# Kernel optimization log

Hardware: AMD Instinct MI355X
Metric: run time of the kernel (lower is better)

Reference implementation:

```python
import jax, jax.numpy as jnp
import numpy as np
import math
jax.config.update('jax_enable_x64', True)

# ---- camera constants (match init_kwargs) ----
WAVELENGTHS = np.array([632e-9, 550e-9, 450e-9])
FOCAL_LENGTH = 50e-3
FOCAL_DEPTH = 1.7
MIN_DEPTH, MAX_DEPTH = 1.0, 5.0
N_DEPTHS = 16
IMAGE_SIZE = 384
MASK_SIZE = 2048
MASK_DIAMETER = 2.5e-3
PIXEL_PITCH = 6.45e-6
BATCH = 2
SENSOR_DIST = 1.0 / (1.0 / FOCAL_LENGTH - 1.0 / FOCAL_DEPTH)
MASK_PITCH = MASK_DIAMETER / MASK_SIZE
EPS = 1e-3


def _j1(x):
    # Bessel J1, Numerical Recipes rational approximation (double precision, ~1e-8 rel err)
    x = np.asarray(x, dtype=np.float64)
    ax = np.abs(x)
    y = x * x
    p1 = x * (72362614232.0 + y * (-7895059235.0 + y * (242396853.1 + y * (-2972611.439 + y * (15704.48260 + y * (-30.16036606))))))
    q1 = 144725228442.0 + y * (2300535178.0 + y * (18583304.74 + y * (99447.43394 + y * (376.9991397 + y))))
    small = p1 / q1
    axs = np.maximum(ax, 1e-300)
    z = 8.0 / axs
    y2 = z * z
    xx = ax - 2.356194491
    p2 = 1.0 + y2 * (0.183105e-2 + y2 * (-0.3516396496e-4 + y2 * (0.2457520174e-5 + y2 * (-0.240337019e-6))))
    q2 = 0.04687499995 + y2 * (-0.2002690873e-3 + y2 * (0.8449199096e-5 + y2 * (-0.88228987e-6 + y2 * 0.105787412e-6)))
    big = np.sqrt(0.636619772 / axs) * (np.cos(xx) * p2 - z * np.sin(xx) * q2) * np.sign(x)
    return np.where(ax < 8.0, small, big)


def _precompute():
    # scene distances: inverse-perspective sampling (ips_to_metric)
    d = np.linspace(0.0, 1.0, N_DEPTHS)
    scene_z = 1.0 / (d * (1.0 / MAX_DEPTH - 1.0 / MIN_DEPTH) + 1.0 / MIN_DEPTH)
    wl = WAVELENGTHS.reshape(-1, 1, 1)
    # --- precompute_H ---
    cy = PIXEL_PITCH * np.arange(1, IMAGE_SIZE // 2 + 1, dtype=np.float64).reshape(-1, 1)
    cx = PIXEL_PITCH * np.arange(1, IMAGE_SIZE // 2 + 1, dtype=np.float64).reshape(1, -1)
    rho_sampling = np.sqrt(cy ** 2 + cx ** 2)[None] / (wl * SENSOR_DIST)  # [3, H/2, W/2]
    rho_grid = math.sqrt(2) * PIXEL_PITCH * (np.arange(-1, IMAGE_SIZE // 2 + 1, dtype=np.float64) + 0.5)
    rho_grid = rho_grid.reshape(1, -1) / (WAVELENGTHS.reshape(-1, 1) * SENSOR_DIST)  # [3, R]
    r = MASK_PITCH * np.linspace(1, MASK_SIZE / 2, MASK_SIZE // 2).reshape(1, -1, 1)  # [1, M, 1]
    rg = rho_grid[:, None, :]  # [3, 1, R]
    denom = 2.0 * np.pi * rg
    safe = np.where(denom == 0.0, 1.0, denom)
    J = np.where(rg == 0.0, 0.5 * r ** 2, r * _j1(denom * r) / safe)  # [3, M, R]
    H = np.concatenate([J[:, 0:1, :], J[:, 1:, :] - J[:, :-1, :]], axis=1)  # [3, M, R]
    # --- pointsource_inputfield1d ---
    z = scene_z.reshape(1, -1, 1)
    rr = MASK_PITCH * np.linspace(1, MASK_SIZE / 2, MASK_SIZE // 2).reshape(1, 1, -1)
    k = 2.0 * np.pi / wl
    sqrt_z_r = np.sqrt(z ** 2 + rr ** 2)
    amp = z / wl / sqrt_z_r ** 2
    amp = amp / amp.max()
    phase = k * (sqrt_z_r - z)
    sqrt_r_d = np.sqrt(FOCAL_DEPTH ** 2 + rr ** 2)
    phase = phase - k * (sqrt_r_d - FOCAL_DEPTH)
    return (jnp.asarray(H), jnp.asarray(rho_grid), jnp.asarray(rho_sampling),
            jnp.asarray(amp), jnp.asarray(phase))


def setup_inputs() -> dict:
    key = jax.random.key(0)
    k1, k2, k3 = jax.random.split(key, 3)
    H, rho_grid, rho_sampling, prop_amplitude, prop_phase = _precompute()
    img = jax.random.uniform(k1, (BATCH, 3, IMAGE_SIZE, IMAGE_SIZE), dtype=jnp.float32)
    depthmap = jax.random.uniform(k2, (BATCH, 1, IMAGE_SIZE, IMAGE_SIZE), dtype=jnp.float32)
    # micron-scale DOE heightmap (learned parameter in the original)
    heightmap1d = jax.random.uniform(k3, (MASK_SIZE // 2,), dtype=jnp.float64) * 1e-6
    return {"img": img, "depthmap": depthmap, "heightmap1d": heightmap1d,
            "prop_amplitude": prop_amplitude, "prop_phase": prop_phase,
            "H": H, "rho_grid": rho_grid, "rho_sampling": rho_sampling,
            "occlusion": 1}


def reference(img, depthmap, heightmap1d, prop_amplitude, prop_phase, H, rho_grid, rho_sampling, occlusion):
    wl = jnp.asarray(WAVELENGTHS).reshape(-1, 1, 1)  # [3,1,1] float64
    # refractive index (Cauchy fit) and heightmap -> phase delay
    n_idx = 1.5375 + 0.00829045 / (wl * 1e6) ** 2 - 0.000211046 / (wl * 1e6) ** 4
    phase = 2.0 * jnp.pi / wl * (n_idx - 1.0) * heightmap1d.reshape(1, 1, -1) + prop_phase  # [3,D,M]
    # 1D PSF via Hankel transform (double precision)
    real = jnp.einsum('wdm,wmr->wdr', prop_amplitude * jnp.cos(phase), H)
    imag = jnp.einsum('wdm,wmr->wdr', prop_amplitude * jnp.sin(phase), H)
    psf1d = (2.0 * jnp.pi / (wl * SENSOR_DIST)) ** 2 * (real ** 2 + imag ** 2)  # [3,D,R]
    # interpolate radial PSF onto the 2D pixel rho grid (per wavelength)
    hh = IMAGE_SIZE // 2
    def interp_wl(grid, vals, samp):  # grid [R], vals [D,R], samp [hh,hh]
        return jax.vmap(lambda v: jnp.interp(samp.reshape(-1), grid, v))(vals)
    psf_rd = jax.vmap(interp_wl)(rho_grid, psf1d, rho_sampling)  # [3,D,hh*hh]
    psf_rd = jnp.maximum(psf_rd, 0.0).astype(jnp.float32).reshape(3, N_DEPTHS, hh, hh)
    # copy_quadruple: mirror quadrant to full image
    q = jnp.concatenate([jnp.flip(psf_rd, axis=-2), psf_rd], axis=-2)
    psf = jnp.concatenate([jnp.flip(q, axis=-1), q], axis=-1)  # [3,D,H,W]
    psf = jnp.fft.fftshift(psf, axes=(-2, -1))[None]  # [1,3,D,H,W]
    psf = psf / jnp.sum(psf, axis=(-2, -1), keepdims=True)  # normalize_psf
    # depthmap -> binary layered depth, volume
    idx = jnp.clip(jnp.floor(depthmap * N_DEPTHS).astype(jnp.int32), 0, N_DEPTHS - 1)  # [B,1,H,W]
    layered = (idx[:, :, None, :, :] == jnp.arange(N_DEPTHS).reshape(1, 1, -1, 1, 1)).astype(jnp.float32)
    volume = layered * img[:, :, None]  # [B,3,D,H,W]
    scale = volume.max()
    volume = volume / scale
    S = volume.shape[-2:]
    Fpsf = jnp.fft.rfft2(psf)
    blur = lambda a: jnp.fft.irfft2(jnp.fft.rfft2(a) * Fpsf, s=S)
    if occlusion:
        blurred_alpha = blur(layered)          # [B,3,D,H,W]
        blurred_volume = blur(volume)
        cumsum_alpha = jnp.flip(jnp.cumsum(jnp.flip(layered, axis=-3), axis=-3), axis=-3)
        blurred_cumsum = blur(cumsum_alpha)
        blurred_volume = blurred_volume / (blurred_cumsum + EPS)
        blurred_alpha = blurred_alpha / (blurred_cumsum + EPS)
        # over_op: front-to-back transmittance
        t = jnp.cumprod(1.0 - blurred_alpha, axis=-3)
        over = jnp.concatenate([jnp.ones_like(t[..., :1, :, :]), t[..., :-1, :, :]], axis=-3)
        captimg = jnp.sum(over * blurred_volume, axis=-3)
    else:
        captimg = jnp.sum(blur(volume), axis=-3)
    return scale * captimg  # [B,3,H,W]
```

## Files before the change

kernel.cpp:

```cpp
#include <hip/hip_runtime.h>
#include <math.h>

#define ND 16
#define NSZ 384
#define NHALF 192
#define NPIX 147456
#define QPIX 36864
#define MS2 1024
#define NG 194
#define EPSV 0.001f

__device__ __forceinline__ double ld64(const void* p, long i, int f){
  return f ? ((const double*)p)[i] : (double)((const float*)p)[i];
}
__device__ __forceinline__ int dtflag(const void* rg){
  double d = ((const double*)rg)[1];
  return (fabs(d) < 1.0e9) ? 1 : 0;
}

__device__ __forceinline__ void init_tws(float* twr, float* twi){
  for (int j=(int)threadIdx.x; j<NSZ; j+=(int)blockDim.x){
    double s,c; sincos((2.0*M_PI/384.0)*(double)j, &s, &c);
    twr[j]=(float)c; twi[j]=(float)(-s);
  }
}

template<int STR,int DIR>
__device__ __forceinline__ void fft384s(float* xr,float* xi,float* yr,float* yi,
                                        int u,const float* twr,const float* twi){
  const float KH = (DIR>0)?0.86602540378443865f:-0.86602540378443865f;
  float *Xr=xr,*Xi=xi,*Yr=yr,*Yi=yi;
  #pragma unroll
  for (int i0=0;i0<128;i0+=64){
    int p=i0+u;
    float ar=Xr[p*STR],ai=Xi[p*STR];
    float br=Xr[(p+128)*STR],bi=Xi[(p+128)*STR];
    float cr=Xr[(p+256)*STR],ci=Xi[(p+256)*STR];
    float t1r=br+cr,t1i=bi+ci;
    float y0r=ar+t1r,y0i=ai+t1i;
    float t2r=ar-0.5f*t1r,t2i=ai-0.5f*t1i;
    float bdr=br-cr,bdi=bi-ci;
    float t3r=KH*bdi,t3i=-KH*bdr;
    float w1r=twr[p],     w1i=(DIR>0)?twi[p]:-twi[p];
    float w2r=twr[2*p],   w2i=(DIR>0)?twi[2*p]:-twi[2*p];
    float y1r=t2r+t3r,y1i=t2i+t3i;
    float y2r=t2r-t3r,y2i=t2i-t3i;
    Yr[(3*p  )*STR]=y0r;             Yi[(3*p  )*STR]=y0i;
    Yr[(3*p+1)*STR]=y1r*w1r-y1i*w1i; Yi[(3*p+1)*STR]=y1r*w1i+y1i*w1r;
    Yr[(3*p+2)*STR]=y2r*w2r-y2i*w2i; Yi[(3*p+2)*STR]=y2r*w2i+y2i*w2r;
  }
  __syncthreads();
  { float*t; t=Xr;Xr=Yr;Yr=t; t=Xi;Xi=Yi;Yi=t; }
  #pragma unroll
  for (int st=0; st<7; st++){
    const int s = 3<<st;
    #pragma unroll
    for (int i0=0;i0<192;i0+=64){
      int i=i0+u, p=i/s, t=p*s;
      float ar=Xr[i*STR],ai=Xi[i*STR];
      float br=Xr[(i+192)*STR],bi=Xi[(i+192)*STR];
      float wr=twr[t], wi=(DIR>0)?twi[t]:-twi[t];
      float sur=ar+br,sui=ai+bi;
      float dr=ar-br,di=ai-bi;
      int o=i+t;
      Yr[o*STR]=sur;             Yi[o*STR]=sui;
      Yr[(o+s)*STR]=dr*wr-di*wi; Yi[(o+s)*STR]=dr*wi+di*wr;
    }
    __syncthreads();
    { float*t2; t2=Xr;Xr=Yr;Yr=t2; t2=Xi;Xi=Yi;Yi=t2; }
  }
}

__global__ __launch_bounds__(256) void k_dotA(const void* __restrict__ h1d,
    const void* __restrict__ amp, const void* __restrict__ pph,
    const void* __restrict__ Hm, const void* __restrict__ rg,
    double2* __restrict__ part){
  int wd = blockIdx.x >> 3, ch = blockIdx.x & 7;
  int w = wd >> 4;
  int f = dtflag(rg);
  int m0 = ch << 7;
  __shared__ double sac[128], sas[128];
  int tid = (int)threadIdx.x;
  if (tid < 128){
    double wl = (w==0) ? 6.32e-07 : (w==1 ? 5.5e-07 : 4.5e-07);
    double um2 = (wl*1e6)*(wl*1e6);
    double n_idx = 1.5375 + 0.00829045/um2 - 0.000211046/(um2*um2);
    double coef = (2.0*M_PI/wl)*(n_idx-1.0);
    long mi = m0 + tid;
    double h = ld64(h1d, mi, f);
    double a = ld64(amp, (long)wd*MS2 + mi, f);
    double p = ld64(pph, (long)wd*MS2 + mi, f);
    double s,c; sincos(coef*h + p, &s, &c);
    sac[tid] = a*c; sas[tid] = a*s;
  }
  __syncthreads();
  int r = tid;
  if (r < NG){
    double sr=0.0, si=0.0;
    if (f){
      const double* Hw = (const double*)Hm + ((size_t)w*MS2 + m0)*NG + r;
      #pragma unroll 4
      for (int m=0;m<128;m++){
        double h = Hw[(size_t)m*NG];
        sr += sac[m]*h; si += sas[m]*h;
      }
    } else {
      const float* Hw = (const float*)Hm + ((size_t)w*MS2 + m0)*NG + r;
      #pragma unroll 4
      for (int m=0;m<128;m++){
        double h = (double)Hw[(size_t)m*NG];
        sr += sac[m]*h; si += sas[m]*h;
      }
    }
    part[(size_t)blockIdx.x*NG + r] = make_double2(sr, si);
  }
}

__global__ __launch_bounds__(256) void k_interp2(const double2* __restrict__ part,
    const void* __restrict__ rg, const void* __restrict__ rs,
    float* __restrict__ q, double* __restrict__ sums_b){
  int wdl = blockIdx.x / 144, blk = blockIdx.x % 144;
  int c = wdl >> 4;
  int pix = blk*256 + (int)threadIdx.x;
  int f = dtflag(rg);
  __shared__ double v[NG];
  int tid = (int)threadIdx.x;
  if (tid < NG){
    double sr=0.0, si=0.0;
    #pragma unroll
    for (int ch=0; ch<8; ch++){
      double2 pp = part[(size_t)(wdl*8+ch)*NG + tid];
      sr += pp.x; si += pp.y;
    }
    v[tid] = sr*sr + si*si;
  }
  __syncthreads();
  long gbase = (long)c*NG;
  double rho = ld64(rs, (long)c*QPIX + pix, f);
  double g0 = ld64(rg, gbase, f);
  double delta = ld64(rg, gbase+1, f) - g0;
  int i = (int)floor((rho-g0)/delta);
  if (i < 0) i = 0; if (i > 192) i = 192;
  double gi  = ld64(rg, gbase+i,   f);
  double gi1 = ld64(rg, gbase+i+1, f);
  if (i > 0  && rho < gi)  { i--; gi1 = gi; gi = ld64(rg, gbase+i, f); }
  else if (i < 192 && rho > gi1){ i++; gi = gi1; gi1 = ld64(rg, gbase+i+1, f); }
  double gl = ld64(rg, gbase+NG-1, f);
  double val;
  if (rho <= g0)      val = v[0];
  else if (rho >= gl) val = v[NG-1];
  else { double t = (rho-gi)/(gi1-gi); val = v[i] + (v[i+1]-v[i])*t; }
  if (val < 0.0) val = 0.0;
  q[(size_t)wdl*QPIX + pix] = (float)val;
  __shared__ double red[256];
  red[threadIdx.x] = val;
  __syncthreads();
  for (int s=128; s>0; s>>=1){
    if ((int)threadIdx.x < s) red[threadIdx.x] += red[threadIdx.x+s];
    __syncthreads();
  }
  if (threadIdx.x==0) atomicAdd(&sums_b[wdl], red[0]);
}

__global__ __launch_bounds__(256) void k_rows_fwd(
    const float* __restrict__ q, const double* __restrict__ sums,
    float* __restrict__ Rr, const float* __restrict__ img,
    const float* __restrict__ depth, float2* __restrict__ V,
    float2* __restrict__ S){
  __shared__ float b0r[NSZ*5], b0i[NSZ*5], b1r[NSZ*5], b1i[NSZ*5];
  __shared__ float twr[NSZ], twi[NSZ];
  init_tws(twr, twi);
  int bi = blockIdx.x;
  int rl = (int)threadIdx.x>>6, u = (int)threadIdx.x&63;
  float *xr=b0r+rl, *xi=b0i+rl, *yr=b1r+rl, *yi=b1i+rl;
  if (bi < 48*24){
    int imgi = bi/24, t = bi%24;
    int y0 = t*8 + 2*rl;
    float sc = (float)(1.0/(4.0*sums[imgi]*147456.0));
    const float* q0 = q + ((size_t)imgi*QPIX + (size_t)y0*NHALF);
    const float* q1 = q0 + NHALF;
    #pragma unroll
    for (int k=0;k<6;k++){
      int x = u+64*k;
      int gx = (x<NHALF)? x : (383-x);
      xr[x*5] = q0[gx]*sc;
      xi[x*5] = q1[gx]*sc;
    }
    __syncthreads();
    fft384s<5,1>(xr,xi,yr,yi,u,twr,twi);
    const float PC=0.86602540378443865f, PS=-0.5f;
    float s0,c0; __sincosf((float)M_PI*(float)u/384.0f,&s0,&c0);
    float phr=c0, phi=-s0;
    float* o0 = Rr + ((size_t)imgi*192 + y0)*NSZ;
    float* o1 = o0 + NSZ;
    #pragma unroll
    for (int k=0;k<6;k++){
      int kx = u+64*k;
      int m  = kx ? (384-kx) : 0;
      float Zr=xr[kx*5], Zi=xi[kx*5], Zmr=xr[m*5], Zmi=xi[m*5];
      float Ar=0.5f*(Zr+Zmr), Ai=0.5f*(Zi-Zmi);
      float Br=0.5f*(Zi+Zmi), Bi=-0.5f*(Zr-Zmr);
      o0[kx] = Ar*phr - Ai*phi;
      o1[kx] = Br*phr - Bi*phi;
      float nr=phr*PC-phi*PS, ni=phr*PS+phi*PC; phr=nr; phi=ni;
    }
  } else if (bi < 48*24 + 48*96){
    int i2 = bi - 48*24;
    int im48 = i2/96, grp = i2%96;
    int c = im48>>4, d = im48&15;
    int y = grp*4 + rl;
    const float* i0 = img + (((size_t)0*3+c)*NPIX + (size_t)y*NSZ);
    const float* i1 = img + (((size_t)1*3+c)*NPIX + (size_t)y*NSZ);
    const float* d0 = depth + (size_t)y*NSZ;
    const float* d1 = depth + (size_t)NPIX + (size_t)y*NSZ;
    #pragma unroll
    for (int k=0;k<6;k++){
      int x=u+64*k;
      int ia=(int)floorf(d0[x]*16.f); ia=ia<0?0:(ia>15?15:ia);
      int ib=(int)floorf(d1[x]*16.f); ib=ib<0?0:(ib>15?15:ib);
      xr[x*5] = (ia==d)? i0[x] : 0.f;
      xi[x*5] = (ib==d)? i1[x] : 0.f;
    }
    __syncthreads();
    fft384s<5,1>(xr,xi,yr,yi,u,twr,twi);
    float2* orow = V + ((size_t)im48*NPIX + (size_t)y*NSZ);
    #pragma unroll
    for (int k=0;k<6;k++){ int x=u+64*k; orow[x]=make_float2(xr[x*5],xi[x*5]); }
  } else {
    int i3 = bi - 48*24 - 48*96;
    int d = i3/96, grp = i3%96;
    int y = grp*4+rl;
    const float* d0 = depth + (size_t)y*NSZ;
    const float* d1 = depth + (size_t)NPIX + (size_t)y*NSZ;
    #pragma unroll
    for (int k=0;k<6;k++){
      int x=u+64*k;
      int ia=(int)floorf(d0[x]*16.f); ia=ia<0?0:(ia>15?15:ia);
      int ib=(int)floorf(d1[x]*16.f); ib=ib<0?0:(ib>15?15:ib);
      xr[x*5]=(ia==d)?1.f:0.f;
      xi[x*5]=(ib==d)?1.f:0.f;
    }
    __syncthreads();
    fft384s<5,1>(xr,xi,yr,yi,u,twr,twi);
    float2* orow = S + ((size_t)d*NPIX + (size_t)y*NSZ);
    #pragma unroll
    for (int k=0;k<6;k++){ int x=u+64*k; orow[x]=make_float2(xr[x*5],xi[x*5]); }
  }
}

__global__ __launch_bounds__(512) void k_colsFS(const float* __restrict__ Rr,
    float* __restrict__ Rc, float2* __restrict__ S){
  __shared__ float b0r[NSZ*9], b0i[NSZ*9], b1r[NSZ*9], b1i[NSZ*9];
  __shared__ float twr[NSZ], twi[NSZ];
  init_tws(twr,twi);
  int bi = blockIdx.x;
  if (bi < 1152){
    int imgi = bi/24, cg = bi%24;
    int j16 = (int)threadIdx.x&15, r0 = (int)threadIdx.x>>4;
    int uu = j16>>1;
    const float* rbase = Rr + (size_t)imgi*192*NSZ + cg*16 + j16;
    #pragma unroll
    for (int k=0;k<12;k++){
      int y = r0 + 32*k;
      int gy = (y<NHALF)? y : (383-y);
      float v = rbase[(size_t)gy*NSZ];
      if (j16&1) b0i[y*9+uu]=v; else b0r[y*9+uu]=v;
    }
    __syncthreads();
    int cc = (int)threadIdx.x>>6, u = (int)threadIdx.x&63;
    fft384s<9,1>(b0r+cc,b0i+cc,b1r+cc,b1i+cc,u,twr,twi);
    const float PC=0.96592582628906829f, PS=-0.25881904510252076f;
    float s0,c0; __sincosf((float)M_PI*(float)r0/384.f,&s0,&c0);
    float phr=c0, phi=-s0;
    float* ob = Rc + (size_t)imgi*NPIX + cg*16 + j16;
    #pragma unroll
    for (int k=0;k<12;k++){
      int ky=r0+32*k;
      int m = ky ? (384-ky) : 0;
      float Zr=b0r[ky*9+uu], Zi=b0i[ky*9+uu], Zmr=b0r[m*9+uu], Zmi=b0i[m*9+uu];
      float Cr,Ci;
      if (j16&1){ Cr=0.5f*(Zi+Zmi); Ci=-0.5f*(Zr-Zmr); }
      else      { Cr=0.5f*(Zr+Zmr); Ci= 0.5f*(Zi-Zmi); }
      ob[(size_t)ky*NSZ] = Cr*phr - Ci*phi;
      float nr=phr*PC-phi*PS, ni=phr*PS+phi*PC; phr=nr; phi=ni;
    }
  } else {
    int i2 = bi - 1152;
    int imgi = i2/48, cg = i2%48;
    size_t boff = (size_t)imgi*NPIX + (size_t)cg*8;
    int j = (int)threadIdx.x&7, r0 = (int)threadIdx.x>>3;
    #pragma unroll
    for (int k=0;k<6;k++){
      int r=r0+64*k;
      float2 v = S[boff + (size_t)r*NSZ + j];
      b0r[r*9+j]=v.x; b0i[r*9+j]=v.y;
    }
    __syncthreads();
    int cc=(int)threadIdx.x>>6, u=(int)threadIdx.x&63;
    fft384s<9,1>(b0r+cc,b0i+cc,b1r+cc,b1i+cc,u,twr,twi);
    #pragma unroll
    for (int k=0;k<6;k++){
      int r=r0+64*k;
      S[boff+(size_t)r*NSZ+j] = make_float2(b0r[r*9+j], b0i[r*9+j]);
    }
  }
}

__global__ __launch_bounds__(512) void k_FM(float2* __restrict__ V,
    const float* __restrict__ Rc, const float2* __restrict__ S,
    float2* __restrict__ L, int nf){
  __shared__ float b0r[NSZ*9], b0i[NSZ*9], b1r[NSZ*9], b1i[NSZ*9];
  __shared__ float twr[NSZ], twi[NSZ];
  init_tws(twr,twi);
  const float PC=0.86602540378443865f, PS=0.5f;
  int bi = blockIdx.x;
  int j = (int)threadIdx.x&7, r0 = (int)threadIdx.x>>3;
  int cc=(int)threadIdx.x>>6, u=(int)threadIdx.x&63;
  if (bi < nf){
    int imgi = bi/48, cg = bi%48;
    size_t boff = (size_t)imgi*NPIX + (size_t)cg*8;
    #pragma unroll
    for (int k=0;k<6;k++){
      int r=r0+64*k;
      float2 v = V[boff + (size_t)r*NSZ + j];
      b0r[r*9+j]=v.x; b0i[r*9+j]=v.y;
    }
    __syncthreads();
    fft384s<9,1>(b0r+cc,b0i+cc,b1r+cc,b1i+cc,u,twr,twi);
    int kx = cg*8+j;
    float s0,c0; __sincosf((float)M_PI*(float)(kx+r0)/384.f,&s0,&c0);
    float phr=c0, phi=s0;
    const float* rb = Rc + (size_t)imgi*NPIX + kx;
    #pragma unroll
    for (int k=0;k<6;k++){
      int r=r0+64*k;
      float R = rb[(size_t)r*NSZ];
      float fr=R*phr, fi=R*phi;
      float br=b0r[r*9+j], bi2=b0i[r*9+j];
      b0r[r*9+j] = br*fr - bi2*fi;
      b0i[r*9+j] = br*fi + bi2*fr;
      float nr=phr*PC-phi*PS, ni=phr*PS+phi*PC; phr=nr; phi=ni;
    }
    __syncthreads();
    fft384s<9,-1>(b0r+cc,b0i+cc,b1r+cc,b1i+cc,u,twr,twi);
    #pragma unroll
    for (int k=0;k<6;k++){
      int r=r0+64*k;
      V[boff+(size_t)r*NSZ+j] = make_float2(b0r[r*9+j], b0i[r*9+j]);
    }
  } else {
    int t = bi - nf;
    int cg = t%48, d=(t/48)&15, c=t/(48*16);
    const float2* src = S  + ((size_t)d*NPIX + (size_t)cg*8);
    const float*  rb  = Rc + ((size_t)(c*ND+d)*NPIX + cg*8);
    float2*       dst = L  + ((size_t)(c*ND+d)*NPIX + (size_t)cg*8);
    int kx = cg*8+j;
    float s0,c0; __sincosf((float)M_PI*(float)(kx+r0)/384.f,&s0,&c0);
    float phr=c0, phi=s0;
    #pragma unroll
    for (int k=0;k<6;k++){
      int r=r0+64*k;
      float2 v = src[(size_t)r*NSZ + j];
      float R = rb[(size_t)r*NSZ + j];
      float fr=R*phr, fi=R*phi;
      b0r[r*9+j] = v.x*fr - v.y*fi;
      b0i[r*9+j] = v.x*fi + v.y*fr;
      float nr=phr*PC-phi*PS, ni=phr*PS+phi*PC; phr=nr; phi=ni;
    }
    __syncthreads();
    fft384s<9,-1>(b0r+cc,b0i+cc,b1r+cc,b1i+cc,u,twr,twi);
    #pragma unroll
    for (int k=0;k<6;k++){
      int r=r0+64*k;
      dst[(size_t)r*NSZ+j] = make_float2(b0r[r*9+j], b0i[r*9+j]);
    }
  }
}

__global__ __launch_bounds__(256) void k_rowsinv(float2* __restrict__ V,
    float2* __restrict__ L){
  __shared__ float b0r[NSZ*5], b0i[NSZ*5], b1r[NSZ*5], b1i[NSZ*5];
  __shared__ float twr[NSZ], twi[NSZ];
  init_tws(twr,twi);
  int bi = blockIdx.x;
  float2* base; int ri;
  if (bi < 4608){ base = V; ri = bi; } else { base = L; ri = bi - 4608; }
  int rl=(int)threadIdx.x>>6, u=(int)threadIdx.x&63;
  float *xr=b0r+rl,*xi=b0i+rl,*yr=b1r+rl,*yi=b1i+rl;
  float2* row = base + ((size_t)ri*4 + rl)*NSZ;
  #pragma unroll
  for (int k=0;k<6;k++){ int x=u+64*k; float2 v=row[x]; xr[x*5]=v.x; xi[x*5]=v.y; }
  __syncthreads();
  fft384s<5,-1>(xr,xi,yr,yi,u,twr,twi);
  #pragma unroll
  for (int k=0;k<6;k++){ int x=u+64*k; row[x]=make_float2(xr[x*5],xi[x*5]); }
}

__global__ __launch_bounds__(256) void k_combine(const float2* __restrict__ L,
    const float2* __restrict__ V, float* __restrict__ out){
  int t = blockIdx.x*256 + (int)threadIdx.x;
  int c = t / (NPIX/2);
  int pp = t - c*(NPIX/2);
  size_t base = (size_t)(c*ND)*NPIX + (size_t)pp*2;
  float A0a=0.f,C0a=0.f,A1a=0.f,C1a=0.f;
  float A0b=0.f,C0b=0.f,A1b=0.f,C1b=0.f;
  for (int d=ND-1; d>=0; --d){
    float4 l = *(const float4*)(L + base + (size_t)d*NPIX);
    float4 v = *(const float4*)(V + base + (size_t)d*NPIX);
    A0a += l.x; A1a += l.y; A0b += l.z; A1b += l.w;
    float ic0a=1.f/(A0a+EPSV), ic1a=1.f/(A1a+EPSV);
    float ic0b=1.f/(A0b+EPSV), ic1b=1.f/(A1b+EPSV);
    C0a = v.x*ic0a + (1.f - l.x*ic0a)*C0a;
    C1a = v.y*ic1a + (1.f - l.y*ic1a)*C1a;
    C0b = v.z*ic0b + (1.f - l.z*ic0b)*C0b;
    C1b = v.w*ic1b + (1.f - l.w*ic1b)*C1b;
  }
  size_t o0 = (size_t)(0*3 + c)*NPIX + (size_t)pp*2;
  size_t o1 = (size_t)(1*3 + c)*NPIX + (size_t)pp*2;
  out[o0]   = C0a; out[o0+1] = C0b;
  out[o1]   = C1a; out[o1+1] = C1b;
}

extern "C" void kernel_launch(void* const* d_in, const int* in_sizes, int n_in,
                              void* d_out, int out_size, void* d_ws, size_t ws_size,
                              hipStream_t stream){
  const float* img   = (const float*)d_in[0];
  const float* depth = (const float*)d_in[1];
  const void*  h1d   = d_in[2];
  const void*  amp   = d_in[3];
  const void*  pph   = d_in[4];
  const void*  Hm    = d_in[5];
  const void*  rg    = d_in[6];
  const void*  rs    = d_in[7];
  float* out = (float*)d_out;
  (void)in_sizes; (void)n_in; (void)out_size;

  char* ws = (char*)d_ws;
  size_t off = 0;
  auto take = [&](size_t b)->char*{ char* p = ws + off; off += (b + 255) & ~(size_t)255; return p; };
  double*  sums = (double*) take((size_t)48*8);
  double2* part = (double2*)take((size_t)48*8*NG*16);
  float*   q    = (float*)  take((size_t)48*QPIX*4);
  float*   Rr   = (float*)  take((size_t)48*192*NSZ*4);
  float*   Rc   = (float*)  take((size_t)48*NPIX*4);
  float2*  V    = (float2*) take((size_t)48*NPIX*8);
  float2*  S    = (float2*) take((size_t)16*NPIX*8);
  float2*  L    = (float2*) take((size_t)48*NPIX*8);
  if (ws_size < off) return;

  hipMemsetAsync(sums, 0, 48*8, stream);
  k_dotA<<<48*8, 256, 0, stream>>>(h1d, amp, pph, Hm, rg, part);
  k_interp2<<<48*144, 256, 0, stream>>>(part, rg, rs, q, sums);
  k_rows_fwd<<<48*24 + 48*96 + 16*96, 256, 0, stream>>>(q, sums, Rr, img, depth, V, S);
  k_colsFS<<<1152 + 16*48, 512, 0, stream>>>(Rr, Rc, S);
  k_FM<<<48*48 + 3*16*48, 512, 0, stream>>>(V, Rc, S, L, 48*48);
  k_rowsinv<<<9216, 256, 0, stream>>>(V, L);
  k_combine<<<864, 256, 0, stream>>>(L, V, out);
}
```

Before: 319.7 us.

## Fuse inverse row FFTs with depth compositing into one kernel

Replaces the separate inverse row-FFT kernel, which wrote V and L back to global memory, and the combine kernel with a single kernel. Each block owns one image row per channel, runs the 16-depth inverse FFTs for L and V in shared memory eight at a time, and composites the depths in registers before writing the output. This drops a full global write and re-read of the V and L volumes plus one launch. In exchange there are far fewer blocks (1152 of 512 threads), larger shared-memory tiles, extra barriers, and threads above 384 sit idle during compositing.

```diff
diff --git a/kernel.cpp b/kernel.cpp
--- a/kernel.cpp
+++ b/kernel.cpp
@@ -377,48 +377,57 @@
   }
 }
 
-__global__ __launch_bounds__(256) void k_rowsinv(float2* __restrict__ V,
-    float2* __restrict__ L){
-  __shared__ float b0r[NSZ*5], b0i[NSZ*5], b1r[NSZ*5], b1i[NSZ*5];
+__global__ __launch_bounds__(512) void k_finish(const float2* __restrict__ V,
+    const float2* __restrict__ L, float* __restrict__ out){
+  __shared__ float b0r[NSZ*9], b0i[NSZ*9], b1r[NSZ*9], b1i[NSZ*9];
   __shared__ float twr[NSZ], twi[NSZ];
   init_tws(twr,twi);
-  int bi = blockIdx.x;
-  float2* base; int ri;
-  if (bi < 4608){ base = V; ri = bi; } else { base = L; ri = bi - 4608; }
-  int rl=(int)threadIdx.x>>6, u=(int)threadIdx.x&63;
-  float *xr=b0r+rl,*xi=b0i+rl,*yr=b1r+rl,*yi=b1i+rl;
-  float2* row = base + ((size_t)ri*4 + rl)*NSZ;
-  #pragma unroll
-  for (int k=0;k<6;k++){ int x=u+64*k; float2 v=row[x]; xr[x*5]=v.x; xi[x*5]=v.y; }
-  __syncthreads();
-  fft384s<5,-1>(xr,xi,yr,yi,u,twr,twi);
-  #pragma unroll
-  for (int k=0;k<6;k++){ int x=u+64*k; row[x]=make_float2(xr[x*5],xi[x*5]); }
-}
-
-__global__ __launch_bounds__(256) void k_combine(const float2* __restrict__ L,
-    const float2* __restrict__ V, float* __restrict__ out){
-  int t = blockIdx.x*256 + (int)threadIdx.x;
-  int c = t / (NPIX/2);
-  int pp = t - c*(NPIX/2);
-  size_t base = (size_t)(c*ND)*NPIX + (size_t)pp*2;
-  float A0a=0.f,C0a=0.f,A1a=0.f,C1a=0.f;
-  float A0b=0.f,C0b=0.f,A1b=0.f,C1b=0.f;
-  for (int d=ND-1; d>=0; --d){
-    float4 l = *(const float4*)(L + base + (size_t)d*NPIX);
-    float4 v = *(const float4*)(V + base + (size_t)d*NPIX);
-    A0a += l.x; A1a += l.y; A0b += l.z; A1b += l.w;
-    float ic0a=1.f/(A0a+EPSV), ic1a=1.f/(A1a+EPSV);
-    float ic0b=1.f/(A0b+EPSV), ic1b=1.f/(A1b+EPSV);
-    C0a = v.x*ic0a + (1.f - l.x*ic0a)*C0a;
-    C1a = v.y*ic1a + (1.f - l.y*ic1a)*C1a;
-    C0b = v.z*ic0b + (1.f - l.z*ic0b)*C0b;
-    C1b = v.w*ic1b + (1.f - l.w*ic1b)*C1b;
-  }
-  size_t o0 = (size_t)(0*3 + c)*NPIX + (size_t)pp*2;
-  size_t o1 = (size_t)(1*3 + c)*NPIX + (size_t)pp*2;
-  out[o0]   = C0a; out[o0+1] = C0b;
-  out[o1]   = C1a; out[o1+1] = C1b;
+  int c = blockIdx.x/NSZ, y = blockIdx.x - c*NSZ;
+  int unit = (int)threadIdx.x>>6, u = (int)threadIdx.x&63;
+  int x = (int)threadIdx.x;
+  size_t rowbase = (size_t)y*NSZ;
+  float A0=0.f,A1=0.f,C0=0.f,C1=0.f;
+  float blr[8], bli[8];
+  for (int half=1; half>=0; --half){
+    int d = half*8 + unit;
+    {
+      const float2* lr = L + ((size_t)(c*ND+d)*NPIX + rowbase);
+      #pragma unroll
+      for (int k=0;k<6;k++){ int x2=u+64*k; float2 v=lr[x2];
+        b0r[x2*9+unit]=v.x; b0i[x2*9+unit]=v.y; }
+      __syncthreads();
+      fft384s<9,-1>(b0r+unit,b0i+unit,b1r+unit,b1i+unit,u,twr,twi);
+      if (x < NSZ){
+        #pragma unroll
+        for (int jj=0;jj<8;jj++){ blr[jj]=b0r[x*9+jj]; bli[jj]=b0i[x*9+jj]; }
+      }
+      __syncthreads();
+    }
+    {
+      const float2* vr = V + ((size_t)(c*ND+d)*NPIX + rowbase);
+      #pragma unroll
+      for (int k=0;k<6;k++){ int x2=u+64*k; float2 v=vr[x2];
+        b0r[x2*9+unit]=v.x; b0i[x2*9+unit]=v.y; }
+      __syncthreads();
+      fft384s<9,-1>(b0r+unit,b0i+unit,b1r+unit,b1i+unit,u,twr,twi);
+      if (x < NSZ){
+        #pragma unroll
+        for (int jj=7;jj>=0;--jj){
+          float bl0=blr[jj], bl1=bli[jj];
+          float v0=b0r[x*9+jj], v1=b0i[x*9+jj];
+          A0 += bl0; A1 += bl1;
+          float ic0=1.f/(A0+EPSV), ic1=1.f/(A1+EPSV);
+          C0 = v0*ic0 + (1.f - bl0*ic0)*C0;
+          C1 = v1*ic1 + (1.f - bl1*ic1)*C1;
+        }
+      }
+      __syncthreads();
+    }
+  }
+  if (x < NSZ){
+    out[(size_t)(0*3+c)*NPIX + rowbase + x] = C0;
+    out[(size_t)(1*3+c)*NPIX + rowbase + x] = C1;
+  }
 }
 
 extern "C" void kernel_launch(void* const* d_in, const int* in_sizes, int n_in,
@@ -454,6 +463,5 @@
   k_rows_fwd<<<48*24 + 48*96 + 16*96, 256, 0, stream>>>(q, sums, Rr, img, depth, V, S);
   k_colsFS<<<1152 + 16*48, 512, 0, stream>>>(Rr, Rc, S);
   k_FM<<<48*48 + 3*16*48, 512, 0, stream>>>(V, Rc, S, L, 48*48);
-  k_rowsinv<<<9216, 256, 0, stream>>>(V, L);
-  k_combine<<<864, 256, 0, stream>>>(L, V, out);
-}
+  k_finish<<<3*NSZ, 512, 0, stream>>>(V, L, out);
+}
```

Result: slower. 339.0 us (+6.0%).
